# Performance work log

Measured on AMD Instinct MI355X. Metric: run time of the kernel, lower is better.

The kernel has to match this reference:

```python
import jax, jax.numpy as jnp
import numpy as np
import math

B, S, HID = 2, 4096, 768
H, D, M = 12, 64, 64  # heads, head_dim, num_landmarks
CK = 33  # conv kernel size


def setup_inputs() -> dict:
    key = jax.random.key(0)
    ks = jax.random.split(key, 4)
    x = jax.random.normal(ks[0], (B, S, HID), dtype=jnp.float32)
    qkv_w = jax.random.normal(ks[1], (3 * HID, HID), dtype=jnp.float32) * 0.02
    qkv_b = jnp.zeros((3 * HID,), dtype=jnp.float32)
    conv_w = jax.random.normal(ks[2], (H, 1, CK, 1), dtype=jnp.float32) * 0.02
    out_w = jax.random.normal(ks[3], (HID, HID), dtype=jnp.float32) * 0.02
    out_b = jnp.zeros((HID,), dtype=jnp.float32)
    return {"x": x, "qkv_w": qkv_w, "qkv_b": qkv_b, "conv_w": conv_w,
            "out_w": out_w, "out_b": out_b}


def iterative_inv(mat, n_iter=6):
    # Newton-Schulz pseudo-inverse on [B,H,M,M]
    I = jnp.eye(mat.shape[-1], dtype=mat.dtype)
    K = mat
    a = jnp.abs(K)
    scale = 1.0 / (jnp.max(jnp.sum(a, axis=-2)) * jnp.max(jnp.sum(a, axis=-1)))
    V = scale * jnp.swapaxes(K, -1, -2)
    for _ in range(n_iter):
        KV = K @ V
        V = 0.25 * V @ (13.0 * I - KV @ (15.0 * I - KV @ (7.0 * I - KV)))
    return V


def reference(x, qkv_w, qkv_b, conv_w, out_w, out_b):
    scale = 1.0 / math.sqrt(D)
    qkv = x @ qkv_w.T + qkv_b  # [B,S,3*HID]
    q, k, v = jnp.split(qkv, 3, axis=-1)
    # [B,H,S,D]
    Q = q.reshape(B, S, H, D).transpose(0, 2, 1, 3)
    K = k.reshape(B, S, H, D).transpose(0, 2, 1, 3)
    V = v.reshape(B, S, H, D).transpose(0, 2, 1, 3)
    # landmark means over contiguous segments of size S//M
    seg = S // M
    Q_l = Q.reshape(B, H, M, seg, D).mean(axis=-2)  # [B,H,M,D]
    K_l = K.reshape(B, H, M, seg, D).mean(axis=-2)
    kernel_1 = jax.nn.softmax(jnp.einsum('bhsd,bhmd->bhsm', Q, K_l) * scale, axis=-1)
    kernel_2 = jax.nn.softmax(jnp.einsum('bhmd,bhnd->bhmn', Q_l, K_l) * scale, axis=-1)
    kernel_3 = jax.nn.softmax(jnp.einsum('bhmd,bhsd->bhms', Q_l, K) * scale, axis=-1)
    X = kernel_1 @ (iterative_inv(kernel_2) @ (kernel_3 @ V))  # [B,H,S,D]
    # depthwise conv over sequence dim: NCHW with C=H, spatial=(S,D), kernel (CK,1)
    pad = CK // 2
    conv_out = jax.lax.conv_general_dilated(
        V, conv_w, window_strides=(1, 1), padding=((pad, pad), (0, 0)),
        dimension_numbers=('NCHW', 'OIHW', 'NCHW'), feature_group_count=H)
    X = X + conv_out
    X = X.transpose(0, 2, 1, 3).reshape(B, S, HID)
    X = X @ out_w.T + out_b
    return X
```

## Files before the change

### kernel.cpp

```cpp
#include <hip/hip_runtime.h>
#include <math.h>

#define B_   2
#define S_   4096
#define HID_ 768
#define H_   12
#define D_   64
#define M_   64
#define CK_  33
#define BH_  (B_*H_)
#define KD_  768
#define NCH_ 32
#define SC_  128

typedef float  f32x4  __attribute__((ext_vector_type(4)));
typedef _Float16 f16x8 __attribute__((ext_vector_type(8)));
typedef unsigned short u16;

__device__ __forceinline__ u16 f2h_bits(float f) {
  union { _Float16 h; u16 u; } c; c.h = (_Float16)f; return c.u;
}
__device__ __forceinline__ float h2f(u16 b) {
  union { _Float16 h; u16 u; } c; c.u = b; return (float)c.h;
}
__device__ __forceinline__ void cvt8_hl(const float4 a, const float4 b,
                                        f16x8* hi, f16x8* lo) {
  const float v[8] = {a.x, a.y, a.z, a.w, b.x, b.y, b.z, b.w};
  f16x8 H, L;
#pragma unroll
  for (int e = 0; e < 8; ++e) {
    const _Float16 hh = (_Float16)v[e];
    H[e] = hh;
    L[e] = (_Float16)(v[e] - (float)hh);
  }
  *hi = H; *lo = L;
}
__device__ __forceinline__ void wsplit(u16* Hh, u16* Hl, int idx, float v) {
  const _Float16 hh = (_Float16)v;
  Hh[idx] = f2h_bits(v);
  Hl[idx] = f2h_bits(v - (float)hh);
}

__device__ __forceinline__ void gld16(const void* g, void* l) {
  __builtin_amdgcn_global_load_lds(
      (const __attribute__((address_space(1))) void*)g,
      (__attribute__((address_space(3))) void*)l, 16, 0, 0);
}

#define N8X  786432
#define N8WQ 221184
#define N8WO 73728
__global__ __launch_bounds__(256) void split3(
    const float* __restrict__ x, const float* __restrict__ qkv_w,
    const float* __restrict__ out_w,
    u16* __restrict__ Xh, u16* __restrict__ Wqh, u16* __restrict__ Woh)
{
  const int i = blockIdx.x * 256 + threadIdx.x;
  const float* src; u16* dst; int j;
  if (i < N8X)                 { src = x;     dst = Xh;  j = i; }
  else if (i < N8X + N8WQ)     { src = qkv_w; dst = Wqh; j = i - N8X; }
  else if (i < N8X + N8WQ + N8WO) { src = out_w; dst = Woh; j = i - N8X - N8WQ; }
  else return;
  const float4 a = ((const float4*)src)[2 * j], b = ((const float4*)src)[2 * j + 1];
  const float v[8] = {a.x, a.y, a.z, a.w, b.x, b.y, b.z, b.w};
  union { u16 u[8]; uint4 q; } hv;
#pragma unroll
  for (int e = 0; e < 8; ++e) hv.u[e] = f2h_bits(v[e]);
  ((uint4*)dst)[j] = hv.q;
}

template<int MODE>
__global__ __launch_bounds__(256) void gemm_wave(
    const u16* __restrict__ Ahg, const u16* __restrict__ Bhg,
    const float* __restrict__ bias,
    float* __restrict__ oF, u16* __restrict__ oQ, u16* __restrict__ oK,
    u16* __restrict__ oV,
    float* __restrict__ Ql, float* __restrict__ Kl, u16* __restrict__ Klh)
{
  constexpr int NBX = (MODE == 0) ? 18 : 6;
  constexpr int NT  = KD_ / 32;
  constexpr int NWG = NBX * 64;
  constexpr int CPX = NWG / 8;

  __shared__ __align__(16) u16 lds[4][2][2][2048];

  const int tid = threadIdx.x;
  const int lin = blockIdx.y * NBX + blockIdx.x;
  const int swb = (lin & 7) * CPX + (lin >> 3);
  const int m0 = (swb / NBX) * 128;
  const int n0 = (swb % NBX) * 128;

  const int wave = tid >> 6, lane = tid & 63;
  const int wm = wave >> 1, wn = wave & 1;
  const int lr = lane & 15, kg = lane >> 4;

  const int srow = lane >> 2;
  const int sk = ((lane & 3) ^ ((lane >> 3) & 3)) * 8;

  const u16* pA = Ahg + (size_t)(m0 + wm * 64 + srow) * KD_ + sk;
  const u16* pB = Bhg + (size_t)(n0 + wn * 64 + srow) * KD_ + sk;

  u16* wbase = &lds[wave][0][0][0];

  f32x4 acc[4][4];
#pragma unroll
  for (int i = 0; i < 4; ++i)
#pragma unroll
    for (int j = 0; j < 4; ++j) acc[i][j] = (f32x4){0.f, 0.f, 0.f, 0.f};

  const int kq = (kg ^ ((lr >> 1) & 3)) * 8;

#define WSTAGE_(buf, kt) do {                                   \
    const size_t go_ = (size_t)(kt) * 32;                       \
    u16* La_ = wbase + (buf) * 4096 + lane * 8;                 \
    u16* Lb_ = La_ + 2048;                                      \
    gld16(pA + go_,              La_);                          \
    gld16(pA + go_ + 16 * KD_,   La_ + 512);                    \
    gld16(pA + go_ + 32 * KD_,   La_ + 1024);                   \
    gld16(pA + go_ + 48 * KD_,   La_ + 1536);                   \
    gld16(pB + go_,              Lb_);                          \
    gld16(pB + go_ + 16 * KD_,   Lb_ + 512);                    \
    gld16(pB + go_ + 32 * KD_,   Lb_ + 1024);                   \
    gld16(pB + go_ + 48 * KD_,   Lb_ + 1536);                   \
  } while (0)

  WSTAGE_(0, 0);

  int cur = 0;
  for (int kt = 0; kt < NT; ++kt) {
    if (kt + 1 < NT) {
      WSTAGE_(cur ^ 1, kt + 1);
      asm volatile("s_waitcnt vmcnt(8)" ::: "memory");
    } else {
      asm volatile("s_waitcnt vmcnt(0)" ::: "memory");
    }
    __builtin_amdgcn_sched_barrier(0);

    const u16* Abuf = wbase + cur * 4096;
    const u16* Bbuf = Abuf + 2048;
    f16x8 af[4], bf[4];
#pragma unroll
    for (int i = 0; i < 4; ++i) af[i] = *(const f16x8*)&Abuf[(i * 16 + lr) * 32 + kq];
#pragma unroll
    for (int j = 0; j < 4; ++j) bf[j] = *(const f16x8*)&Bbuf[(j * 16 + lr) * 32 + kq];
#pragma unroll
    for (int i = 0; i < 4; ++i)
#pragma unroll
      for (int j = 0; j < 4; ++j)
        acc[i][j] = __builtin_amdgcn_mfma_f32_16x16x32_f16(af[i], bf[j], acc[i][j], 0, 0, 0);

    cur ^= 1;
  }
#undef WSTAGE_

  if (MODE == 0) {
    const int part = n0 / 768;
    const int within0 = n0 + wn * 64 - part * 768;
    const int h0 = within0 >> 6;
    u16* base = (part == 0) ? oQ : ((part == 1) ? oK : oV);
#pragma unroll
    for (int i = 0; i < 4; ++i) {
      const int mbase = m0 + wm * 64 + i * 16 + kg * 4;
#pragma unroll
      for (int j = 0; j < 4; ++j) {
        const int d = j * 16 + lr;
        const float bv = bias[n0 + wn * 64 + d];
#pragma unroll
        for (int r = 0; r < 4; ++r) {
          const int row = mbase + r;
          const int b = row >> 12, s = row & (S_ - 1);
          base[(((size_t)(b * H_ + h0) * S_ + s) << 6) + d] = f2h_bits(acc[i][j][r] + bv);
        }
      }
    }
    if (part < 2) {
      const int rowseg = m0 + wm * 64;
      const int b = rowseg >> 12;
      const int seg = (rowseg & (S_ - 1)) >> 6;
      const int bhh = b * H_ + h0;
      float* dst = (part == 0) ? Ql : Kl;
#pragma unroll
      for (int j = 0; j < 4; ++j) {
        float sj = 0.f;
#pragma unroll
        for (int i = 0; i < 4; ++i)
#pragma unroll
          for (int r = 0; r < 4; ++r) sj += acc[i][j][r];
        sj += __shfl_xor(sj, 16);
        sj += __shfl_xor(sj, 32);
        if (kg == 0) {
          const int d = j * 16 + lr;
          const float lm = sj * (1.f / 64.f) + bias[n0 + wn * 64 + d];
          dst[((size_t)bhh * M_ + seg) * 64 + d] = lm;
          if (part == 1) Klh[((size_t)bhh * M_ + seg) * 64 + d] = f2h_bits(lm);
        }
      }
    }
  } else {
#pragma unroll
    for (int i = 0; i < 4; ++i) {
      const int mbase = m0 + wm * 64 + i * 16 + kg * 4;
#pragma unroll
      for (int j = 0; j < 4; ++j) {
        const int ncol = n0 + wn * 64 + j * 16 + lr;
        const float bv = bias[ncol];
#pragma unroll
        for (int r = 0; r < 4; ++r) {
          const int row = mbase + r;
          oF[(size_t)row * HID_ + ncol] = acc[i][j][r] + bv;
        }
      }
    }
  }
}

__global__ __launch_bounds__(256) void kernel2_softmax(
    const float* __restrict__ Ql, const float* __restrict__ Kl,
    float* __restrict__ K2, float* __restrict__ colmax, float* __restrict__ rowmax)
{
  __shared__ float Qs[64][68], Ks[64][68], S2[64][68];
  __shared__ float red1[64], red2[64];
  const int bh = blockIdx.x, tid = threadIdx.x;
  for (int idx = tid; idx < 4096; idx += 256) {
    const int r = idx >> 6, c = idx & 63;
    Qs[r][c] = Ql[(size_t)bh * 4096 + idx];
    Ks[r][c] = Kl[(size_t)bh * 4096 + idx];
  }
  __syncthreads();
  for (int idx = tid; idx < 4096; idx += 256) {
    const int r = idx >> 6, c = idx & 63;
    float dot = 0.f;
#pragma unroll
    for (int k = 0; k < 64; k += 4) {
      const float4 a = *(const float4*)&Qs[r][k];
      const float4 b = *(const float4*)&Ks[c][k];
      dot += a.x * b.x + a.y * b.y + a.z * b.z + a.w * b.w;
    }
    S2[r][c] = dot * 0.125f;
  }
  __syncthreads();
  if (tid < 64) {
    const int r = tid;
    float mx = -1e30f;
    for (int c = 0; c < 64; ++c) mx = fmaxf(mx, S2[r][c]);
    float sum = 0.f;
    for (int c = 0; c < 64; ++c) { const float e = expf(S2[r][c] - mx); S2[r][c] = e; sum += e; }
    const float inv = 1.f / sum;
    for (int c = 0; c < 64; ++c) S2[r][c] *= inv;
  }
  __syncthreads();
  for (int idx = tid; idx < 4096; idx += 256)
    K2[(size_t)bh * 4096 + idx] = S2[idx >> 6][idx & 63];
  if (tid < 64) {
    float cs = 0.f, rs = 0.f;
    for (int m = 0; m < 64; ++m) { cs += S2[m][tid]; rs += S2[tid][m]; }
    red1[tid] = cs; red2[tid] = rs;
  }
  __syncthreads();
  if (tid == 0) {
    float mc = 0.f, mr = 0.f;
    for (int i = 0; i < 64; ++i) { mc = fmaxf(mc, red1[i]); mr = fmaxf(mr, red2[i]); }
    colmax[bh] = mc; rowmax[bh] = mr;
  }
}

#define NST 88
__device__ __forceinline__ void mfma64x64(
    const u16* Ah, const u16* Al, const u16* Bh, const u16* Bl,
    int wave, int lr, int kg, f32x4 C[4])
{
#pragma unroll
  for (int j = 0; j < 4; ++j) C[j] = (f32x4){0.f, 0.f, 0.f, 0.f};
#pragma unroll
  for (int kk = 0; kk < 2; ++kk) {
    const int ao = (wave * 16 + lr) * NST + kk * 32 + kg * 8;
    const f16x8 ah = *(const f16x8*)&Ah[ao];
    const f16x8 al = *(const f16x8*)&Al[ao];
#pragma unroll
    for (int j = 0; j < 4; ++j) {
      const int bo = (j * 16 + lr) * NST + kk * 32 + kg * 8;
      const f16x8 bh = *(const f16x8*)&Bh[bo];
      const f16x8 bl = *(const f16x8*)&Bl[bo];
      C[j] = __builtin_amdgcn_mfma_f32_16x16x32_f16(ah, bh, C[j], 0, 0, 0);
      C[j] = __builtin_amdgcn_mfma_f32_16x16x32_f16(ah, bl, C[j], 0, 0, 0);
      C[j] = __builtin_amdgcn_mfma_f32_16x16x32_f16(al, bh, C[j], 0, 0, 0);
    }
  }
}

__global__ __launch_bounds__(256) void newton_combine(
    const float* __restrict__ K2, const float* __restrict__ colmax,
    const float* __restrict__ rowmax,
    const float* __restrict__ Opart, const float* __restrict__ mpart,
    const float* __restrict__ lpart, float* __restrict__ W2)
{
  __shared__ __align__(16) u16 K2h[64*NST], K2l[64*NST];
  __shared__ __align__(16) u16 Vh_[64*NST], Vl_[64*NST];
  __shared__ __align__(16) u16 VTh[64*NST], VTl[64*NST];
  __shared__ __align__(16) u16 KVh[64*NST], KVl[64*NST];
  __shared__ __align__(16) u16 TTh[64*NST], TTl[64*NST];
  __shared__ float w_[64][33];
  __shared__ float scale_s;

  const int bh = blockIdx.x, tid = threadIdx.x;
  const int wave = tid >> 6, lane = tid & 63;
  const int lr = lane & 15, kg = lane >> 4;

  if (tid == 0) {
    float mc = 0.f, mr = 0.f;
    for (int i = 0; i < BH_; ++i) { mc = fmaxf(mc, colmax[i]); mr = fmaxf(mr, rowmax[i]); }
    scale_s = 1.f / (mc * mr);
  }
  __syncthreads();
  const float scale = scale_s;

  for (int idx = tid; idx < 4096; idx += 256) {
    const int r = idx >> 6, c = idx & 63;
    const float v = K2[(size_t)bh * 4096 + idx];
    wsplit(K2h, K2l, r * NST + c, v);
    const float sv = scale * v;
    wsplit(VTh, VTl, r * NST + c, sv);
    wsplit(Vh_, Vl_, c * NST + r, sv);
  }
  __syncthreads();

  f32x4 C[4];
  for (int it = 0; it < 6; ++it) {
    mfma64x64(K2h, K2l, VTh, VTl, wave, lr, kg, C);
#pragma unroll
    for (int j = 0; j < 4; ++j)
#pragma unroll
      for (int r = 0; r < 4; ++r) {
        const int row = wave * 16 + kg * 4 + r, col = j * 16 + lr;
        const float kv = C[j][r];
        wsplit(KVh, KVl, row * NST + col, kv);
        wsplit(TTh, TTl, col * NST + row, (row == col ? 7.f : 0.f) - kv);
      }
    __syncthreads();
    mfma64x64(KVh, KVl, TTh, TTl, wave, lr, kg, C);
    __syncthreads();
#pragma unroll
    for (int j = 0; j < 4; ++j)
#pragma unroll
      for (int r = 0; r < 4; ++r) {
        const int row = wave * 16 + kg * 4 + r, col = j * 16 + lr;
        wsplit(TTh, TTl, col * NST + row, (row == col ? 15.f : 0.f) - C[j][r]);
      }
    __syncthreads();
    mfma64x64(KVh, KVl, TTh, TTl, wave, lr, kg, C);
    __syncthreads();
#pragma unroll
    for (int j = 0; j < 4; ++j)
#pragma unroll
      for (int r = 0; r < 4; ++r) {
        const int row = wave * 16 + kg * 4 + r, col = j * 16 + lr;
        wsplit(TTh, TTl, col * NST + row, (row == col ? 13.f : 0.f) - C[j][r]);
      }
    __syncthreads();
    mfma64x64(Vh_, Vl_, TTh, TTl, wave, lr, kg, C);
#pragma unroll
    for (int j = 0; j < 4; ++j)
#pragma unroll
      for (int r = 0; r < 4; ++r) {
        const int row = wave * 16 + kg * 4 + r, col = j * 16 + lr;
        const float v = 0.25f * C[j][r];
        wsplit(Vh_, Vl_, row * NST + col, v);
        wsplit(VTh, VTl, col * NST + row, v);
      }
    __syncthreads();
  }

  if (tid < 64) {
    const int m = tid;
    float Mx = -1e30f;
    for (int j = 0; j < NCH_; ++j)
      Mx = fmaxf(Mx, mpart[((size_t)bh * NCH_ + j) * 64 + m]);
    float denom = 0.f;
    for (int j = 0; j < NCH_; ++j)
      denom += expf(mpart[((size_t)bh * NCH_ + j) * 64 + m] - Mx) *
               lpart[((size_t)bh * NCH_ + j) * 64 + m];
    const float inv = 1.f / denom;
    for (int j = 0; j < NCH_; ++j)
      w_[m][j] = expf(mpart[((size_t)bh * NCH_ + j) * 64 + m] - Mx) * inv;
  }
  __syncthreads();
  u16* W1Th = K2h;
  u16* W1Tl = K2l;
  {
    const int mg = tid >> 4, dq = (tid & 15) * 4;
#pragma unroll
    for (int i = 0; i < 4; ++i) {
      const int m = mg * 4 + i;
      float4 acc = make_float4(0.f, 0.f, 0.f, 0.f);
      for (int j = 0; j < NCH_; ++j) {
        const float ww = w_[m][j];
        const float4 o = *(const float4*)&Opart[(((size_t)bh * NCH_ + j) * 64 + m) * 64 + dq];
        acc.x += ww * o.x; acc.y += ww * o.y; acc.z += ww * o.z; acc.w += ww * o.w;
      }
      wsplit(W1Th, W1Tl, (dq + 0) * NST + m, acc.x);
      wsplit(W1Th, W1Tl, (dq + 1) * NST + m, acc.y);
      wsplit(W1Th, W1Tl, (dq + 2) * NST + m, acc.z);
      wsplit(W1Th, W1Tl, (dq + 3) * NST + m, acc.w);
    }
  }
  __syncthreads();
  mfma64x64(Vh_, Vl_, W1Th, W1Tl, wave, lr, kg, C);
#pragma unroll
  for (int j = 0; j < 4; ++j)
#pragma unroll
    for (int r = 0; r < 4; ++r) {
      const int row = wave * 16 + kg * 4 + r, col = j * 16 + lr;
      W2[(size_t)bh * 4096 + row * 64 + col] = C[j][r];
    }
}

__global__ __launch_bounds__(256) void k3v_pass1(
    const float* __restrict__ Ql, const u16* __restrict__ Kh,
    const u16* __restrict__ Vh, float* __restrict__ Opart,
    float* __restrict__ mpart, float* __restrict__ lpart)
{
  __shared__ float P[64][129];
  __shared__ float red1[64][4], red2[64][4];

  const int ch = blockIdx.x;
  const int bh = blockIdx.y;
  const int tid = threadIdx.x;
  const int wave = tid >> 6, lane = tid & 63;
  const int lr = lane & 15, kg = lane >> 4;

  const float* Qlb = Ql + (size_t)bh * 4096;
  const u16*   Kb  = Kh + (size_t)bh * S_ * 64;
  const u16*   Vb  = Vh + (size_t)bh * S_ * 64;

  f16x8 ah[4][2], al[4][2];
#pragma unroll
  for (int mt = 0; mt < 4; ++mt)
#pragma unroll
    for (int kk = 0; kk < 2; ++kk) {
      const float* qr = Qlb + (size_t)(mt * 16 + lr) * 64 + kk * 32 + kg * 8;
      cvt8_hl(*(const float4*)qr, *(const float4*)(qr + 4), &ah[mt][kk], &al[mt][kk]);
    }

#pragma unroll
  for (int t = 0; t < 2; ++t) {
    const int s0 = (wave * 2 + t) * 16;
    const int srow = ch * SC_ + s0 + lr;
    f32x4 acc[4];
#pragma unroll
    for (int mt = 0; mt < 4; ++mt) acc[mt] = (f32x4){0.f, 0.f, 0.f, 0.f};
#pragma unroll
    for (int kk = 0; kk < 2; ++kk) {
      const f16x8 bhf = *(const f16x8*)&Kb[(size_t)srow * 64 + kk * 32 + kg * 8];
#pragma unroll
      for (int mt = 0; mt < 4; ++mt) {
        acc[mt] = __builtin_amdgcn_mfma_f32_16x16x32_f16(ah[mt][kk], bhf, acc[mt], 0, 0, 0);
        acc[mt] = __builtin_amdgcn_mfma_f32_16x16x32_f16(al[mt][kk], bhf, acc[mt], 0, 0, 0);
      }
    }
#pragma unroll
    for (int mt = 0; mt < 4; ++mt)
#pragma unroll
      for (int r = 0; r < 4; ++r)
        P[mt * 16 + kg * 4 + r][s0 + lr] = acc[mt][r] * 0.125f;
  }
  __syncthreads();

  const int r = tid >> 2, q = tid & 3;
  {
    float mx = -1e30f;
#pragma unroll
    for (int s = 0; s < 32; ++s) mx = fmaxf(mx, P[r][q * 32 + s]);
    red1[r][q] = mx;
  }
  __syncthreads();
  const float rowmax = fmaxf(fmaxf(red1[r][0], red1[r][1]),
                             fmaxf(red1[r][2], red1[r][3]));
  {
    float sum = 0.f;
#pragma unroll
    for (int s = 0; s < 32; ++s) {
      const float e = expf(P[r][q * 32 + s] - rowmax);
      P[r][q * 32 + s] = e;
      sum += e;
    }
    red2[r][q] = sum;
  }
  __syncthreads();
  if (q == 0) {
    const float rowsum = red2[r][0] + red2[r][1] + red2[r][2] + red2[r][3];
    mpart[((size_t)bh * NCH_ + ch) * 64 + r] = rowmax;
    lpart[((size_t)bh * NCH_ + ch) * 64 + r] = rowsum;
  }

  const int mg = tid >> 4, dq = (tid & 15) * 4;
  float4 oacc[4];
#pragma unroll
  for (int i = 0; i < 4; ++i) oacc[i] = make_float4(0.f, 0.f, 0.f, 0.f);
  for (int s = 0; s < SC_; ++s) {
    const ushort4 vv = *(const ushort4*)&Vb[(size_t)(ch * SC_ + s) * 64 + dq];
    const float4 v = make_float4(h2f(vv.x), h2f(vv.y), h2f(vv.z), h2f(vv.w));
#pragma unroll
    for (int i = 0; i < 4; ++i) {
      const float p = P[mg * 4 + i][s];
      oacc[i].x += p * v.x; oacc[i].y += p * v.y;
      oacc[i].z += p * v.z; oacc[i].w += p * v.w;
    }
  }
#pragma unroll
  for (int i = 0; i < 4; ++i) {
    const size_t o = (((size_t)bh * NCH_ + ch) * 64 + mg * 4 + i) * 64 + dq;
    *(float4*)&Opart[o] = oacc[i];
  }
}

__global__ __launch_bounds__(256) void attn_conv_fused(
    const u16* __restrict__ Qh, const u16* __restrict__ Klh,
    const float* __restrict__ W2, const u16* __restrict__ Vh,
    const float* __restrict__ cw, u16* __restrict__ Xch)
{
  __shared__ __align__(16) u16 smem[19456];
  __shared__ float cws[33];

  const int ch = blockIdx.x;
  const int bh = blockIdx.y;
  const int tid = threadIdx.x;
  const int wave = tid >> 6, lane = tid & 63;
  const int lr = lane & 15, kg = lane >> 4;
  const int b = bh / H_, h = bh % H_;
  const int s0 = ch * 128;

  u16* Ph   = smem;
  u16* W2Th = smem + 9728;
  u16* W2Tl = smem + 14592;

  if (tid < 33) cws[tid] = cw[h * 33 + tid];
  for (int idx = tid; idx < 4096; idx += 256) {
    const int m = idx >> 6, d = idx & 63;
    const float w = W2[(size_t)bh * 4096 + idx];
    const _Float16 hh = (_Float16)w;
    W2Th[d * 76 + m] = f2h_bits(w);
    W2Tl[d * 76 + m] = f2h_bits(w - (float)hh);
  }

  const u16* Klb = Klh + (size_t)bh * 4096;
  const u16* Qb  = Qh + (size_t)bh * S_ * 64;
  f16x8 bf[4][2];
#pragma unroll
  for (int nt = 0; nt < 4; ++nt)
#pragma unroll
    for (int kk = 0; kk < 2; ++kk)
      bf[nt][kk] = *(const f16x8*)&Klb[(size_t)(nt * 16 + lr) * 64 + kk * 32 + kg * 8];

  f32x4 sacc[2][4];
#pragma unroll
  for (int t = 0; t < 2; ++t) {
#pragma unroll
    for (int nt = 0; nt < 4; ++nt) sacc[t][nt] = (f32x4){0.f, 0.f, 0.f, 0.f};
    const int rloc = wave * 32 + t * 16;
    f16x8 af[2];
#pragma unroll
    for (int kk = 0; kk < 2; ++kk)
      af[kk] = *(const f16x8*)&Qb[(size_t)(s0 + rloc + lr) * 64 + kk * 32 + kg * 8];
#pragma unroll
    for (int kk = 0; kk < 2; ++kk)
#pragma unroll
      for (int nt = 0; nt < 4; ++nt)
        sacc[t][nt] = __builtin_amdgcn_mfma_f32_16x16x32_f16(af[kk], bf[nt][kk], sacc[t][nt], 0, 0, 0);
  }

#pragma unroll
  for (int t = 0; t < 2; ++t)
#pragma unroll
    for (int nt = 0; nt < 4; ++nt)
      sacc[t][nt] *= 0.125f;

  float rinv[2][4];
#pragma unroll
  for (int t = 0; t < 2; ++t) {
#pragma unroll
    for (int r = 0; r < 4; ++r) {
      float mx = fmaxf(fmaxf(sacc[t][0][r], sacc[t][1][r]),
                       fmaxf(sacc[t][2][r], sacc[t][3][r]));
      mx = fmaxf(mx, __shfl_xor(mx, 1));
      mx = fmaxf(mx, __shfl_xor(mx, 2));
      mx = fmaxf(mx, __shfl_xor(mx, 4));
      mx = fmaxf(mx, __shfl_xor(mx, 8));
      float sum = 0.f;
#pragma unroll
      for (int nt = 0; nt < 4; ++nt) {
        const float e = expf(sacc[t][nt][r] - mx);
        sacc[t][nt][r] = e;
        sum += e;
      }
      sum += __shfl_xor(sum, 1);
      sum += __shfl_xor(sum, 2);
      sum += __shfl_xor(sum, 4);
      sum += __shfl_xor(sum, 8);
      rinv[t][r] = 1.f / sum;
    }
  }

#pragma unroll
  for (int t = 0; t < 2; ++t)
#pragma unroll
    for (int nt = 0; nt < 4; ++nt)
#pragma unroll
      for (int r = 0; r < 4; ++r) {
        const int row = wave * 32 + t * 16 + kg * 4 + r;
        Ph[row * 76 + nt * 16 + lr] = f2h_bits(sacc[t][nt][r] * rinv[t][r]);
      }
  __syncthreads();

  f32x4 oacc[2][4];
#pragma unroll
  for (int t = 0; t < 2; ++t)
#pragma unroll
    for (int dt = 0; dt < 4; ++dt) oacc[t][dt] = (f32x4){0.f, 0.f, 0.f, 0.f};
#pragma unroll
  for (int kk = 0; kk < 2; ++kk) {
    f16x8 pa[2];
#pragma unroll
    for (int t = 0; t < 2; ++t)
      pa[t] = *(const f16x8*)&Ph[(wave * 32 + t * 16 + lr) * 76 + kk * 32 + kg * 8];
#pragma unroll
    for (int dt = 0; dt < 4; ++dt) {
      const f16x8 wh = *(const f16x8*)&W2Th[(dt * 16 + lr) * 76 + kk * 32 + kg * 8];
      const f16x8 wl = *(const f16x8*)&W2Tl[(dt * 16 + lr) * 76 + kk * 32 + kg * 8];
#pragma unroll
      for (int t = 0; t < 2; ++t) {
        oacc[t][dt] = __builtin_amdgcn_mfma_f32_16x16x32_f16(pa[t], wh, oacc[t][dt], 0, 0, 0);
        oacc[t][dt] = __builtin_amdgcn_mfma_f32_16x16x32_f16(pa[t], wl, oacc[t][dt], 0, 0, 0);
      }
    }
  }
  __syncthreads();

  float* O = (float*)smem;
#pragma unroll
  for (int t = 0; t < 2; ++t)
#pragma unroll
    for (int dt = 0; dt < 4; ++dt)
#pragma unroll
      for (int r = 0; r < 4; ++r) {
        const int row = wave * 32 + t * 16 + kg * 4 + r;
        O[row * 68 + dt * 16 + lr] = oacc[t][dt][r];
      }
  __syncthreads();

  const int d = tid & 63, rg = tid >> 6;
  const int rbase = s0 + rg * 32;
  const u16* Vd = Vh + (size_t)bh * S_ * 64 + d;

  float v[40];
#pragma unroll
  for (int j = 0; j < 40; ++j) {
    const int sv = rbase - 16 + j;
    v[j] = (sv >= 0 && sv < S_) ? h2f(Vd[(size_t)sv * 64]) : 0.f;
  }

#pragma clang loop unroll(disable)
  for (int c = 0; c < 4; ++c) {
#pragma unroll
    for (int rr = 0; rr < 8; ++rr) {
      float acc = 0.f;
#pragma unroll
      for (int t = 0; t < 33; ++t) acc += v[rr + t] * cws[t];
      const int row = rg * 32 + c * 8 + rr;
      const float oo = O[row * 68 + d] + acc;
      const size_t idx = ((size_t)(b * S_ + s0 + row)) * HID_ + h * 64 + d;
      Xch[idx] = f2h_bits(oo);
    }
    if (c < 3) {
#pragma unroll
      for (int j = 0; j < 32; ++j) v[j] = v[j + 8];
#pragma unroll
      for (int j = 0; j < 8; ++j) {
        const int sv = rbase + 24 + c * 8 + j;
        v[32 + j] = (sv >= 0 && sv < S_) ? h2f(Vd[(size_t)sv * 64]) : 0.f;
      }
    }
  }
}

extern "C" void kernel_launch(void* const* d_in, const int* in_sizes, int n_in,
                              void* d_out, int out_size, void* d_ws, size_t ws_size,
                              hipStream_t stream)
{
  (void)in_sizes; (void)n_in; (void)out_size; (void)ws_size;
  const float* x      = (const float*)d_in[0];
  const float* qkv_w  = (const float*)d_in[1];
  const float* qkv_b  = (const float*)d_in[2];
  const float* conv_w = (const float*)d_in[3];
  const float* out_w  = (const float*)d_in[4];
  const float* out_b  = (const float*)d_in[5];
  float* out = (float*)d_out;

  float* ws = (float*)d_ws;
  u16* Qh = (u16*)ws;
  u16* Kh = Qh + 6291456;
  u16* Vh = Kh + 6291456;
  float* Ql = ws + 9437184;
  float* Kl = Ql + 98304;
  float* K2 = Kl + 98304;
  float* W2 = K2 + 98304;
  float* colmax = W2 + 98304;
  float* rowmax = colmax + 32;
  u16* Klh = (u16*)(rowmax + 32);
  float* nxt = rowmax + 32 + 49152;
  u16* Xh  = (u16*)nxt;
  u16* Xl  = Xh + 6291456;
  u16* Wqh = Xl + 6291456;
  u16* Woh = Wqh + 1769472;
  u16* Xch = Xh;
  float* Opart = (float*)Xh;
  float* mpart = (float*)Xl;
  float* lpart = mpart + BH_ * NCH_ * 64;

  split3<<<(N8X + N8WQ + N8WO + 255) / 256, 256, 0, stream>>>(
      x, qkv_w, out_w, Xh, Wqh, Woh);

  gemm_wave<0><<<dim3(18, 64), 256, 0, stream>>>(
      Xh, Wqh, qkv_b, nullptr, Qh, Kh, Vh, Ql, Kl, Klh);

  kernel2_softmax<<<BH_, 256, 0, stream>>>(Ql, Kl, K2, colmax, rowmax);

  k3v_pass1<<<dim3(NCH_, BH_), 256, 0, stream>>>(Ql, Kh, Vh, Opart, mpart, lpart);

  newton_combine<<<BH_, 256, 0, stream>>>(K2, colmax, rowmax,
                                          Opart, mpart, lpart, W2);

  attn_conv_fused<<<dim3(NCH_, BH_), 256, 0, stream>>>(
      Qh, Klh, W2, Vh, conv_w, Xch);

  gemm_wave<1><<<dim3(6, 64), 256, 0, stream>>>(
      Xch, Woh, out_b, out, nullptr, nullptr, nullptr,
      nullptr, nullptr, nullptr);
}
```

Baseline: 211.7 us.

## Load GEMM MFMA fragments directly from global into registers, dropping LDS staging

Both GEMMs (the QKV projection and the output projection) now read their f16 A/B MFMA fragments straight from global memory into registers. The old path staged tiles through per-wave LDS buffers with global_load_lds. Two register fragment sets are software double-buffered across k-steps. This removes LDS traffic, the swizzle math and the explicit waitcnt handling. The cost is 16-byte strided global loads per lane that rely on L1/L2 for reuse, and higher register pressure.

```diff
diff --git a/kernel.cpp b/kernel.cpp
--- a/kernel.cpp
+++ b/kernel.cpp
@@ -39,12 +39,6 @@
   const _Float16 hh = (_Float16)v;
   Hh[idx] = f2h_bits(v);
   Hl[idx] = f2h_bits(v - (float)hh);
-}
-
-__device__ __forceinline__ void gld16(const void* g, void* l) {
-  __builtin_amdgcn_global_load_lds(
-      (const __attribute__((address_space(1))) void*)g,
-      (__attribute__((address_space(3))) void*)l, 16, 0, 0);
 }
 
 #define N8X  786432
@@ -70,7 +64,7 @@
 }
 
 template<int MODE>
-__global__ __launch_bounds__(256) void gemm_wave(
+__global__ __launch_bounds__(256) void gemm_reg(
     const u16* __restrict__ Ahg, const u16* __restrict__ Bhg,
     const float* __restrict__ bias,
     float* __restrict__ oF, u16* __restrict__ oQ, u16* __restrict__ oK,
@@ -82,8 +76,6 @@
   constexpr int NWG = NBX * 64;
   constexpr int CPX = NWG / 8;
 
-  __shared__ __align__(16) u16 lds[4][2][2][2048];
-
   const int tid = threadIdx.x;
   const int lin = blockIdx.y * NBX + blockIdx.x;
   const int swb = (lin & 7) * CPX + (lin >> 3);
@@ -94,13 +86,8 @@
   const int wm = wave >> 1, wn = wave & 1;
   const int lr = lane & 15, kg = lane >> 4;
 
-  const int srow = lane >> 2;
-  const int sk = ((lane & 3) ^ ((lane >> 3) & 3)) * 8;
-
-  const u16* pA = Ahg + (size_t)(m0 + wm * 64 + srow) * KD_ + sk;
-  const u16* pB = Bhg + (size_t)(n0 + wn * 64 + srow) * KD_ + sk;
-
-  u16* wbase = &lds[wave][0][0][0];
+  const u16* pA = Ahg + (size_t)(m0 + wm * 64 + lr) * KD_ + kg * 8;
+  const u16* pB = Bhg + (size_t)(n0 + wn * 64 + lr) * KD_ + kg * 8;
 
   f32x4 acc[4][4];
 #pragma unroll
@@ -108,50 +95,37 @@
 #pragma unroll
     for (int j = 0; j < 4; ++j) acc[i][j] = (f32x4){0.f, 0.f, 0.f, 0.f};
 
-  const int kq = (kg ^ ((lr >> 1) & 3)) * 8;
-
-#define WSTAGE_(buf, kt) do {                                   \
-    const size_t go_ = (size_t)(kt) * 32;                       \
-    u16* La_ = wbase + (buf) * 4096 + lane * 8;                 \
-    u16* Lb_ = La_ + 2048;                                      \
-    gld16(pA + go_,              La_);                          \
-    gld16(pA + go_ + 16 * KD_,   La_ + 512);                    \
-    gld16(pA + go_ + 32 * KD_,   La_ + 1024);                   \
-    gld16(pA + go_ + 48 * KD_,   La_ + 1536);                   \
-    gld16(pB + go_,              Lb_);                          \
-    gld16(pB + go_ + 16 * KD_,   Lb_ + 512);                    \
-    gld16(pB + go_ + 32 * KD_,   Lb_ + 1024);                   \
-    gld16(pB + go_ + 48 * KD_,   Lb_ + 1536);                   \
+  f16x8 a0[4], b0[4], a1[4], b1[4];
+
+#define LDFRAG(ad, bd, kt_) do {                                         \
+    _Pragma("unroll")                                                    \
+    for (int q_ = 0; q_ < 4; ++q_) {                                     \
+      ad[q_] = *(const f16x8*)&pA[(size_t)(q_ * 16) * KD_ + (kt_) * 32]; \
+      bd[q_] = *(const f16x8*)&pB[(size_t)(q_ * 16) * KD_ + (kt_) * 32]; \
+    }                                                                    \
   } while (0)
 
-  WSTAGE_(0, 0);
-
-  int cur = 0;
-  for (int kt = 0; kt < NT; ++kt) {
-    if (kt + 1 < NT) {
-      WSTAGE_(cur ^ 1, kt + 1);
-      asm volatile("s_waitcnt vmcnt(8)" ::: "memory");
-    } else {
-      asm volatile("s_waitcnt vmcnt(0)" ::: "memory");
-    }
-    __builtin_amdgcn_sched_barrier(0);
-
-    const u16* Abuf = wbase + cur * 4096;
-    const u16* Bbuf = Abuf + 2048;
-    f16x8 af[4], bf[4];
-#pragma unroll
-    for (int i = 0; i < 4; ++i) af[i] = *(const f16x8*)&Abuf[(i * 16 + lr) * 32 + kq];
-#pragma unroll
-    for (int j = 0; j < 4; ++j) bf[j] = *(const f16x8*)&Bbuf[(j * 16 + lr) * 32 + kq];
-#pragma unroll
-    for (int i = 0; i < 4; ++i)
-#pragma unroll
-      for (int j = 0; j < 4; ++j)
-        acc[i][j] = __builtin_amdgcn_mfma_f32_16x16x32_f16(af[i], bf[j], acc[i][j], 0, 0, 0);
-
-    cur ^= 1;
-  }
-#undef WSTAGE_
+#define DOMM(av, bv) do {                                                \
+    _Pragma("unroll")                                                    \
+    for (int i_ = 0; i_ < 4; ++i_)                                       \
+      _Pragma("unroll")                                                  \
+      for (int j_ = 0; j_ < 4; ++j_)                                     \
+        acc[i_][j_] = __builtin_amdgcn_mfma_f32_16x16x32_f16(            \
+            av[i_], bv[j_], acc[i_][j_], 0, 0, 0);                       \
+  } while (0)
+
+  LDFRAG(a0, b0, 0);
+  LDFRAG(a1, b1, 1);
+  for (int kt = 0; kt < NT - 2; kt += 2) {
+    DOMM(a0, b0);
+    LDFRAG(a0, b0, kt + 2);
+    DOMM(a1, b1);
+    LDFRAG(a1, b1, kt + 3);
+  }
+  DOMM(a0, b0);
+  DOMM(a1, b1);
+#undef LDFRAG
+#undef DOMM
 
   if (MODE == 0) {
     const int part = n0 / 768;
@@ -719,7 +693,7 @@
   split3<<<(N8X + N8WQ + N8WO + 255) / 256, 256, 0, stream>>>(
       x, qkv_w, out_w, Xh, Wqh, Woh);
 
-  gemm_wave<0><<<dim3(18, 64), 256, 0, stream>>>(
+  gemm_reg<0><<<dim3(18, 64), 256, 0, stream>>>(
       Xh, Wqh, qkv_b, nullptr, Qh, Kh, Vh, Ql, Kl, Klh);
 
   kernel2_softmax<<<BH_, 256, 0, stream>>>(Ql, Kl, K2, colmax, rowmax);
@@ -732,7 +706,7 @@
   attn_conv_fused<<<dim3(NCH_, BH_), 256, 0, stream>>>(
       Qh, Klh, W2, Vh, conv_w, Xch);
 
-  gemm_wave<1><<<dim3(6, 64), 256, 0, stream>>>(
+  gemm_reg<1><<<dim3(6, 64), 256, 0, stream>>>(
       Xch, Woh, out_b, out, nullptr, nullptr, nullptr,
       nullptr, nullptr, nullptr);
 }
```

Result: slower. 289.4 us (+36.7%).
